# Performance work log

Hardware: AMD Instinct MI355X
Metric: run time of the kernel (lower is better)

Reference implementation:

```python
import jax, jax.numpy as jnp
import numpy as np

B, C, T = 64, 1, 262144
NUM_BANDS = 6
# (min, max) for each of the 18 normalized control params: 6 bands x (gain_dB, cutoff_Hz, Q)
PARAM_RANGES = np.array([
    [-24.0, 24.0], [20.0, 200.0], [0.1, 10.0],      # low shelf
    [-24.0, 24.0], [200.0, 2000.0], [0.1, 10.0],    # band 1
    [-24.0, 24.0], [200.0, 2000.0], [0.1, 10.0],    # band 2
    [-24.0, 24.0], [2000.0, 8000.0], [0.1, 10.0],   # band 3
    [-24.0, 24.0], [4000.0, 12000.0], [0.1, 10.0],  # band 4
    [-24.0, 24.0], [4000.0, 12000.0], [0.1, 10.0],  # high shelf
], dtype=np.float32)
FILTER_TYPES = ["low_shelf", "peaking", "peaking", "peaking", "peaking", "high_shelf"]


def biquad_coeffs(gain_dB, cutoff, q, sr, ftype):
    # Audio-EQ-cookbook biquad coefficients; all inputs shape (B,)
    A = 10.0 ** (gain_dB / 40.0)
    w0 = 2.0 * jnp.pi * (cutoff / sr)
    alpha = jnp.sin(w0) / (2.0 * q)
    c = jnp.cos(w0)
    sA = jnp.sqrt(A)
    if ftype == "low_shelf":
        b0 = A * ((A + 1) - (A - 1) * c + 2 * sA * alpha)
        b1 = 2 * A * ((A - 1) - (A + 1) * c)
        b2 = A * ((A + 1) - (A - 1) * c - 2 * sA * alpha)
        a0 = (A + 1) + (A - 1) * c + 2 * sA * alpha
        a1 = -2 * ((A - 1) + (A + 1) * c)
        a2 = (A + 1) + (A - 1) * c - 2 * sA * alpha
    elif ftype == "high_shelf":
        b0 = A * ((A + 1) + (A - 1) * c + 2 * sA * alpha)
        b1 = -2 * A * ((A - 1) + (A + 1) * c)
        b2 = A * ((A + 1) + (A - 1) * c - 2 * sA * alpha)
        a0 = (A + 1) - (A - 1) * c + 2 * sA * alpha
        a1 = 2 * ((A - 1) - (A + 1) * c)
        a2 = (A + 1) - (A - 1) * c - 2 * sA * alpha
    else:  # peaking
        b0 = 1 + alpha * A
        b1 = -2 * c
        b2 = 1 - alpha * A
        a0 = 1 + alpha / A
        a1 = -2 * c
        a2 = 1 - alpha / A
    bcoef = jnp.stack([b0, b1, b2], axis=-1) / a0[..., None]  # (B, 3)
    acoef = jnp.stack([a0, a1, a2], axis=-1) / a0[..., None]  # (B, 3)
    return bcoef, acoef


def cascade_biquads(x, bcoefs, acoefs):
    # x: (N, T); bcoefs/acoefs: (6, N, 3). Fused cascade of 6 biquads,
    # direct form II transposed, single scan over time.
    def step(state, xt):  # state: (6, N, 2); xt: (N,)
        v = xt
        new_states = []
        for k in range(NUM_BANDS):
            bk, ak = bcoefs[k], acoefs[k]
            s1, s2 = state[k, :, 0], state[k, :, 1]
            y = bk[:, 0] * v + s1
            ns1 = bk[:, 1] * v - ak[:, 1] * y + s2
            ns2 = bk[:, 2] * v - ak[:, 2] * y
            new_states.append(jnp.stack([ns1, ns2], axis=-1))
            v = y
        return jnp.stack(new_states, axis=0), v
    init = jnp.zeros((NUM_BANDS, x.shape[0], 2), dtype=x.dtype)
    _, y = jax.lax.scan(step, init, x.T)  # y: (T, N)
    return y.T


def setup_inputs() -> dict:
    key = jax.random.key(0)
    k1, k2, k3 = jax.random.split(key, 3)
    x = jax.random.normal(k1, (B, C, T), dtype=jnp.float32) * 0.1
    p = jax.random.normal(k2, (B, 22), dtype=jnp.float32)
    W = jax.random.normal(k3, (18, 22), dtype=jnp.float32) * (1.0 / np.sqrt(22.0))
    b = jnp.zeros((18,), dtype=jnp.float32)
    return {"x": x, "p": p, "W": W, "b": b, "sample_rate": 24000}


def reference(x, p, W, b, sample_rate):
    bs, chs, s = x.shape
    sr = jnp.float32(sample_rate)
    # control path: linear + sigmoid -> 18 normalized params in [0, 1]
    pn = jax.nn.sigmoid(p @ W.T + b)  # (bs, 18)
    lo = jnp.asarray(PARAM_RANGES[:, 0])
    hi = jnp.asarray(PARAM_RANGES[:, 1])
    params = pn * (hi - lo) + lo  # denormalized, (bs, 18)
    bcoefs, acoefs = [], []
    for k, ftype in enumerate(FILTER_TYPES):
        g, f, q = params[:, 3 * k], params[:, 3 * k + 1], params[:, 3 * k + 2]
        bk, ak = biquad_coeffs(g, f, q, sr, ftype)
        bcoefs.append(bk)
        acoefs.append(ak)
    bcoefs = jnp.stack(bcoefs, axis=0)  # (6, bs, 3)
    acoefs = jnp.stack(acoefs, axis=0)
    # share each item's EQ across its channels
    bcoefs = jnp.repeat(bcoefs, chs, axis=1)  # (6, bs*chs, 3)
    acoefs = jnp.repeat(acoefs, chs, axis=1)
    y = cascade_biquads(x.reshape(bs * chs, s), bcoefs, acoefs)
    return y.reshape(bs, chs, s)
```

## Files before the change

kernel.cpp:

```cpp
#include <hip/hip_runtime.h>
#include <math.h>

#define NB    64
#define NT    262144
#define CH    64
#define NCK   (NT/CH)
#define NBANDS 6

#define COEF_OFF 0
#define MAT_OFF  4096
#define T_OFF    (MAT_OFF + NB*1728)
#define WPRE_OFF (T_OFF + NB*64*12)
#define D_OFF    (WPRE_OFF + NB*64*12)

struct Coef { float b0, b1, b2, a1, a2; };

__device__ __forceinline__ float rfl(float x) {
  return __int_as_float(__builtin_amdgcn_readfirstlane(__float_as_int(x)));
}

__device__ __forceinline__ float cascade_step(float v, float s[12], const Coef cf[NBANDS]) {
#pragma unroll
  for (int k = 0; k < NBANDS; ++k) {
    float s1 = s[2*k], s2 = s[2*k+1];
    float y   = fmaf(cf[k].b0, v, s1);
    float ns1 = fmaf(cf[k].b1, v, fmaf(-cf[k].a1, y, s2));
    float ns2 = fmaf(cf[k].b2, v, -cf[k].a2 * y);
    s[2*k]   = ns1;
    s[2*k+1] = ns2;
    v = y;
  }
  return v;
}

__device__ __forceinline__ void load_coefs(const float* ws, int batch, Coef cf[NBANDS]) {
  const float* c = ws + COEF_OFF + batch*30;
#pragma unroll
  for (int k = 0; k < NBANDS; ++k) {
    cf[k].b0 = rfl(c[5*k+0]); cf[k].b1 = rfl(c[5*k+1]); cf[k].b2 = rfl(c[5*k+2]);
    cf[k].a1 = rfl(c[5*k+3]); cf[k].a2 = rfl(c[5*k+4]);
  }
}

__global__ __launch_bounds__(64) void k_prep(const float* __restrict__ p, const float* __restrict__ W,
                                             const float* __restrict__ bias, const int* __restrict__ srp,
                                             float* __restrict__ ws) {
  __shared__ float prmS[18];
  __shared__ float cfS[30];
  __shared__ float M0[144], M1[144];
  int b = blockIdx.x, tid = threadIdx.x;
  const float lo[18] = {-24.f,20.f,0.1f,  -24.f,200.f,0.1f,  -24.f,200.f,0.1f,
                        -24.f,2000.f,0.1f, -24.f,4000.f,0.1f, -24.f,4000.f,0.1f};
  const float hi[18] = { 24.f,200.f,10.f,  24.f,2000.f,10.f,  24.f,2000.f,10.f,
                         24.f,8000.f,10.f, 24.f,12000.f,10.f, 24.f,12000.f,10.f};
  if (tid < 18) {
    float acc = bias[tid];
    for (int j = 0; j < 22; ++j) acc = fmaf(W[tid*22+j], p[b*22+j], acc);
    float sg = 1.f / (1.f + expf(-acc));
    prmS[tid] = sg * (hi[tid] - lo[tid]) + lo[tid];
  }
  __syncthreads();
  if (tid < 6) {
    int k = tid;
    float g = prmS[3*k], f = prmS[3*k+1], q = prmS[3*k+2];
    float sr = (float)srp[0];
    float A  = powf(10.f, g * (1.f/40.f));
    float w0 = 6.28318530717958647692f * (f / sr);
    float al = sinf(w0) / (2.f*q);
    float c  = cosf(w0);
    float sA = sqrtf(A);
    float b0,b1,b2,a0,a1,a2;
    if (k == 0) {
      b0 = A*((A+1.f) - (A-1.f)*c + 2.f*sA*al);
      b1 = 2.f*A*((A-1.f) - (A+1.f)*c);
      b2 = A*((A+1.f) - (A-1.f)*c - 2.f*sA*al);
      a0 = (A+1.f) + (A-1.f)*c + 2.f*sA*al;
      a1 = -2.f*((A-1.f) + (A+1.f)*c);
      a2 = (A+1.f) + (A-1.f)*c - 2.f*sA*al;
    } else if (k == 5) {
      b0 = A*((A+1.f) + (A-1.f)*c + 2.f*sA*al);
      b1 = -2.f*A*((A-1.f) + (A+1.f)*c);
      b2 = A*((A+1.f) + (A-1.f)*c - 2.f*sA*al);
      a0 = (A+1.f) - (A-1.f)*c + 2.f*sA*al;
      a1 = 2.f*((A-1.f) - (A+1.f)*c);
      a2 = (A+1.f) - (A-1.f)*c - 2.f*sA*al;
    } else {
      b0 = 1.f + al*A;
      b1 = -2.f*c;
      b2 = 1.f - al*A;
      a0 = 1.f + al/A;
      a1 = -2.f*c;
      a2 = 1.f - al/A;
    }
    float inv = 1.f/a0;
    float* cws = ws + COEF_OFF + b*30;
    cws[5*k+0] = cfS[5*k+0] = b0*inv;
    cws[5*k+1] = cfS[5*k+1] = b1*inv;
    cws[5*k+2] = cfS[5*k+2] = b2*inv;
    cws[5*k+3] = cfS[5*k+3] = a1*inv;
    cws[5*k+4] = cfS[5*k+4] = a2*inv;
  }
  __syncthreads();

  Coef cf[NBANDS];
#pragma unroll
  for (int k = 0; k < NBANDS; ++k) {
    cf[k].b0 = cfS[5*k+0]; cf[k].b1 = cfS[5*k+1]; cf[k].b2 = cfS[5*k+2];
    cf[k].a1 = cfS[5*k+3]; cf[k].a2 = cfS[5*k+4];
  }
  if (tid < 12) {
    float s[12];
#pragma unroll
    for (int r = 0; r < 12; ++r) s[r] = (r == tid) ? 1.f : 0.f;
    cascade_step(0.f, s, cf);
#pragma unroll
    for (int r = 0; r < 12; ++r) M0[r*12 + tid] = s[r];
  }
  __syncthreads();

  float w[12];
#pragma unroll
  for (int r = 0; r < 12; ++r) w[r] = 0.f;
  cascade_step(1.f, w, cf);
  int e63 = 63 - tid;

  float* S = M0; float* D = M1;
  float* mout = ws + MAT_OFF + (size_t)b*1728;
  for (int q = 0; q < 6; ++q) {
    if ((e63 >> q) & 1) {
      float t[12];
#pragma unroll
      for (int r = 0; r < 12; ++r) {
        float acc = 0.f;
#pragma unroll
        for (int k = 0; k < 12; ++k) acc = fmaf(S[r*12+k], w[k], acc);
        t[r] = acc;
      }
#pragma unroll
      for (int r = 0; r < 12; ++r) w[r] = t[r];
    }
    for (int e = tid; e < 144; e += 64) {
      int r = e/12, c = e%12;
      float acc = 0.f;
#pragma unroll
      for (int k = 0; k < 12; ++k) acc = fmaf(S[r*12+k], S[k*12+c], acc);
      D[e] = acc;
    }
    __syncthreads();
    float* t = S; S = D; D = t;
  }
  {
    float* vout = ws + WPRE_OFF + (size_t)b*768;
#pragma unroll
    for (int r = 0; r < 12; ++r) vout[tid*12 + r] = w[r];
  }
  for (int e = tid; e < 144; e += 64) mout[e] = S[e];
  for (int l = 1; l < 12; ++l) {
    for (int e = tid; e < 144; e += 64) {
      int r = e/12, c = e%12;
      float acc = 0.f;
#pragma unroll
      for (int k = 0; k < 12; ++k) acc = fmaf(S[r*12+k], S[k*12+c], acc);
      D[e] = acc;
    }
    __syncthreads();
    float* t = S; S = D; D = t;
    for (int e = tid; e < 144; e += 64) mout[l*144 + e] = S[e];
  }
}

__global__ __launch_bounds__(256, 4) void k_passA(const float* __restrict__ x,
                                                  const float* __restrict__ Vt,
                                                  float* __restrict__ ws) {
  __shared__ float KM[6][144];
  int tid = threadIdx.x, wib = tid >> 6, lane = tid & 63;
  int gw = blockIdx.x*4 + wib;
  int batch = gw >> 6, wv = gw & 63;
  int batch_b = blockIdx.x >> 4;

  const float* mb = ws + MAT_OFF + (size_t)batch_b*1728;
  for (int e = tid; e < 864; e += 256) KM[e/144][e%144] = mb[e];
  __syncthreads();

  const float4* xp = (const float4*)x + (size_t)batch*65536 + (size_t)wv*1024 + (size_t)lane*16;
  const float* Vb = Vt + (size_t)batch_b*768;

  int ph = ((wib << 2) + blockIdx.x) & 15;

  float4 bufs[4];
#pragma unroll
  for (int k = 0; k < 4; ++k) bufs[k] = xp[(ph + k) & 15];

  float s[12];
#pragma unroll
  for (int r = 0; r < 12; ++r) s[r] = 0.f;

#pragma unroll
  for (int j = 0; j < 16; ++j) {
    float4 xv = bufs[j & 3];
    if (j < 12) bufs[j & 3] = xp[(ph + j + 4) & 15];
    int ko = __builtin_amdgcn_readfirstlane(((ph + j) & 15) * 48);
    const float* vr = Vb + ko;
#pragma unroll
    for (int r = 0; r < 12; ++r) {
      float acc = s[r];
      acc = fmaf(vr[r],      xv.x, acc);
      acc = fmaf(vr[12 + r], xv.y, acc);
      acc = fmaf(vr[24 + r], xv.z, acc);
      acc = fmaf(vr[36 + r], xv.w, acc);
      s[r] = acc;
    }
  }

#pragma unroll
  for (int l = 0; l < 6; ++l) {
    const int pd = 1 << l;
    float nb[12];
#pragma unroll
    for (int r = 0; r < 12; ++r) nb[r] = __shfl_up(s[r], pd);
    if (lane >= pd) {
#pragma unroll
      for (int r = 0; r < 12; ++r) {
        float acc = s[r];
#pragma unroll
        for (int c = 0; c < 12; ++c) acc = fmaf(KM[l][r*12+c], nb[c], acc);
        s[r] = acc;
      }
    }
  }

  if (lane == 63) {
    float4* tp = (float4*)(ws + T_OFF + ((size_t)batch*64 + wv)*12);
    tp[0] = make_float4(s[0], s[1], s[2],  s[3]);
    tp[1] = make_float4(s[4], s[5], s[6],  s[7]);
    tp[2] = make_float4(s[8], s[9], s[10], s[11]);
  }

  float e[12];
#pragma unroll
  for (int r = 0; r < 12; ++r) e[r] = __shfl_up(s[r], 1);
  if (lane == 0) {
#pragma unroll
    for (int r = 0; r < 12; ++r) e[r] = 0.f;
  }
  int chunk = wv*64 + lane;
  float4* dp = (float4*)(ws + D_OFF + ((size_t)batch*NCK + chunk)*12);
  dp[0] = make_float4(e[0], e[1], e[2],  e[3]);
  dp[1] = make_float4(e[4], e[5], e[6],  e[7]);
  dp[2] = make_float4(e[8], e[9], e[10], e[11]);
}

__global__ __launch_bounds__(64) void k_scanW(float* __restrict__ ws) {
  __shared__ float WM[6][144];
  int b = blockIdx.x, lane = threadIdx.x;
  const float* mb = ws + MAT_OFF + (size_t)b*1728 + 864;
  for (int e = lane; e < 864; e += 64) WM[e/144][e%144] = mb[e];
  __syncthreads();

  const float4* tp = (const float4*)(ws + T_OFF + ((size_t)b*64 + lane)*12);
  float4 a0 = tp[0], a1 = tp[1], a2 = tp[2];
  float s[12] = {a0.x,a0.y,a0.z,a0.w, a1.x,a1.y,a1.z,a1.w, a2.x,a2.y,a2.z,a2.w};

#pragma unroll
  for (int l = 0; l < 6; ++l) {
    const int pd = 1 << l;
    float nb[12];
#pragma unroll
    for (int r = 0; r < 12; ++r) nb[r] = __shfl_up(s[r], pd);
    if (lane >= pd) {
#pragma unroll
      for (int r = 0; r < 12; ++r) {
        float acc = s[r];
#pragma unroll
        for (int c = 0; c < 12; ++c) acc = fmaf(WM[l][r*12+c], nb[c], acc);
        s[r] = acc;
      }
    }
  }
  float e[12];
#pragma unroll
  for (int r = 0; r < 12; ++r) e[r] = __shfl_up(s[r], 1);
  if (lane == 0) {
#pragma unroll
    for (int r = 0; r < 12; ++r) e[r] = 0.f;
  }
  float4* wp = (float4*)(ws + WPRE_OFF + ((size_t)b*64 + lane)*12);
  wp[0] = make_float4(e[0], e[1], e[2],  e[3]);
  wp[1] = make_float4(e[4], e[5], e[6],  e[7]);
  wp[2] = make_float4(e[8], e[9], e[10], e[11]);
}

__global__ __launch_bounds__(256) void k_passB(const float* __restrict__ x, const float* __restrict__ ws,
                                               float* __restrict__ out) {
  __shared__ float4 buf[4][2][256];
  __shared__ float KM[6][144];
  int tid = threadIdx.x, wib = tid >> 6, lane = tid & 63;
  int gw = blockIdx.x*4 + wib;
  int batch = gw >> 6, wv = gw & 63;
  int batch_b = blockIdx.x >> 4;

  const float* mb = ws + MAT_OFF + (size_t)batch_b*1728;
  for (int e = tid; e < 864; e += 256) KM[e/144][e%144] = mb[e];
  __syncthreads();

  const float4* x4 = (const float4*)x;
  float4* out4 = (float4*)out;
  size_t gbase4 = (size_t)batch*65536 + (size_t)wv*1024;
  int r2 = lane >> 2, c2 = lane & 3;
  float4* bufA = buf[wib][0];
  float4* bufB = buf[wib][1];

  float4 va[4], vb[4];
#pragma unroll
  for (int j = 0; j < 4; ++j) va[j] = x4[gbase4 + (size_t)(j*16 + r2)*16 + c2];

  Coef cf[NBANDS];
  load_coefs(ws, batch, cf);

  int chunk = wv*64 + lane;
  const float4* dp = (const float4*)(ws + D_OFF + ((size_t)batch*NCK + chunk)*12);
  float4 e0 = dp[0], e1 = dp[1], e2 = dp[2];
  const float4* wp = (const float4*)(ws + WPRE_OFF + ((size_t)batch*64 + wv)*12);
  float4 w0 = wp[0], w1 = wp[1], w2 = wp[2];
  float R[12] = {w0.x,w0.y,w0.z,w0.w, w1.x,w1.y,w1.z,w1.w, w2.x,w2.y,w2.z,w2.w};
#pragma unroll
  for (int l = 0; l < 6; ++l) {
    float t[12];
#pragma unroll
    for (int r = 0; r < 12; ++r) {
      float acc = 0.f;
#pragma unroll
      for (int c = 0; c < 12; ++c) acc = fmaf(KM[l][r*12+c], R[c], acc);
      t[r] = acc;
    }
    bool sel = (lane >> l) & 1;
#pragma unroll
    for (int r = 0; r < 12; ++r) R[r] = sel ? t[r] : R[r];
  }
  float s[12] = {e0.x+R[0], e0.y+R[1], e0.z+R[2],  e0.w+R[3],
                 e1.x+R[4], e1.y+R[5], e1.z+R[6],  e1.w+R[7],
                 e2.x+R[8], e2.y+R[9], e2.z+R[10], e2.w+R[11]};

#pragma unroll
  for (int j = 0; j < 4; ++j) bufA[c2*64 + j*16 + r2] = va[j];
  asm volatile("s_waitcnt lgkmcnt(0)" ::: "memory");

#pragma unroll
  for (int q = 0; q < 4; ++q) {
    float4* bp = (q & 1) ? bufB : bufA;
    float4* bn = (q & 1) ? bufA : bufB;
    float4* vr = (q & 1) ? va : vb;
    if (q < 3) {
#pragma unroll
      for (int j = 0; j < 4; ++j)
        vr[j] = x4[gbase4 + (size_t)(j*16 + r2)*16 + (q+1)*4 + c2];
    }
#pragma unroll
    for (int t = 0; t < 4; ++t) {
      float4 xv = bp[t*64 + lane];
      float4 yv;
      yv.x = cascade_step(xv.x, s, cf);
      yv.y = cascade_step(xv.y, s, cf);
      yv.z = cascade_step(xv.z, s, cf);
      yv.w = cascade_step(xv.w, s, cf);
      bp[t*64 + lane] = yv;
    }
    asm volatile("s_waitcnt lgkmcnt(0)" ::: "memory");
#pragma unroll
    for (int j = 0; j < 4; ++j) {
      float4 w = bp[c2*64 + j*16 + r2];
      out4[gbase4 + (size_t)(j*16 + r2)*16 + q*4 + c2] = w;
    }
    if (q < 3) {
#pragma unroll
      for (int j = 0; j < 4; ++j) bn[c2*64 + j*16 + r2] = vr[j];
      asm volatile("s_waitcnt lgkmcnt(0)" ::: "memory");
    }
  }
}

extern "C" void kernel_launch(void* const* d_in, const int* in_sizes, int n_in,
                              void* d_out, int out_size, void* d_ws, size_t ws_size,
                              hipStream_t stream) {
  const float* x    = (const float*)d_in[0];
  const float* p    = (const float*)d_in[1];
  const float* W    = (const float*)d_in[2];
  const float* bias = (const float*)d_in[3];
  const int*   sr   = (const int*)d_in[4];
  float* ws  = (float*)d_ws;
  float* out = (float*)d_out;

  int passBlocks = (NB * NCK) / 256;
  hipLaunchKernelGGL(k_prep,  dim3(NB),         dim3(64),  0, stream, p, W, bias, sr, ws);
  hipLaunchKernelGGL(k_passA, dim3(passBlocks), dim3(256), 0, stream, x, ws + WPRE_OFF, ws);
  hipLaunchKernelGGL(k_scanW, dim3(NB),         dim3(64),  0, stream, ws);
  hipLaunchKernelGGL(k_passB, dim3(passBlocks), dim3(256), 0, stream, x, ws, out);
}
```

Before: 98.32 us.

## Fold warp-level scan into passB and stream passA input via global_load_lds ring

Removes the separate k_scanW launch: each passB wavefront redoes the 64-lane 12x12 matrix prefix scan over the per-warp totals and picks its predecessor's prefix with a shuffle. This needs the second half of the matrix table in LDS. passA now streams its input through a per-wave LDS ring filled by direct global-to-LDS loads, with explicit vmcnt waits, instead of a rotated-phase register buffer. The intent is to save one kernel launch and its dependency gap and to deepen load pipelining, at the cost of redundant scan arithmetic in every passB wave and more LDS per block.

Measured after the change: 101.5 us. 1.03x slower.

```diff
diff --git a/kernel.cpp b/kernel.cpp
--- a/kernel.cpp
+++ b/kernel.cpp
@@ -10,13 +10,26 @@
 #define COEF_OFF 0
 #define MAT_OFF  4096
 #define T_OFF    (MAT_OFF + NB*1728)
-#define WPRE_OFF (T_OFF + NB*64*12)
-#define D_OFF    (WPRE_OFF + NB*64*12)
+#define V_OFF    (T_OFF + NB*64*12)
+#define D_OFF    (V_OFF + NB*64*12)
 
 struct Coef { float b0, b1, b2, a1, a2; };
 
 __device__ __forceinline__ float rfl(float x) {
   return __int_as_float(__builtin_amdgcn_readfirstlane(__float_as_int(x)));
+}
+
+__device__ __forceinline__ void wait_vmcnt(int n) {
+  switch (n) {
+    case 0: asm volatile("s_waitcnt vmcnt(0)" ::: "memory"); break;
+    case 1: asm volatile("s_waitcnt vmcnt(1)" ::: "memory"); break;
+    case 2: asm volatile("s_waitcnt vmcnt(2)" ::: "memory"); break;
+    case 3: asm volatile("s_waitcnt vmcnt(3)" ::: "memory"); break;
+    case 4: asm volatile("s_waitcnt vmcnt(4)" ::: "memory"); break;
+    case 5: asm volatile("s_waitcnt vmcnt(5)" ::: "memory"); break;
+    case 6: asm volatile("s_waitcnt vmcnt(6)" ::: "memory"); break;
+    default: asm volatile("s_waitcnt vmcnt(7)" ::: "memory"); break;
+  }
 }
 
 __device__ __forceinline__ float cascade_step(float v, float s[12], const Coef cf[NBANDS]) {
@@ -150,7 +163,7 @@
     float* t = S; S = D; D = t;
   }
   {
-    float* vout = ws + WPRE_OFF + (size_t)b*768;
+    float* vout = ws + V_OFF + (size_t)b*768;
 #pragma unroll
     for (int r = 0; r < 12; ++r) vout[tid*12 + r] = w[r];
   }
@@ -173,6 +186,7 @@
                                                   const float* __restrict__ Vt,
                                                   float* __restrict__ ws) {
   __shared__ float KM[6][144];
+  __shared__ float4 ring[4][8][64];
   int tid = threadIdx.x, wib = tid >> 6, lane = tid & 63;
   int gw = blockIdx.x*4 + wib;
   int batch = gw >> 6, wv = gw & 63;
@@ -182,25 +196,31 @@
   for (int e = tid; e < 864; e += 256) KM[e/144][e%144] = mb[e];
   __syncthreads();
 
-  const float4* xp = (const float4*)x + (size_t)batch*65536 + (size_t)wv*1024 + (size_t)lane*16;
+  const float4* xg = (const float4*)x + (size_t)batch*65536 + (size_t)wv*1024 + (size_t)lane*16;
   const float* Vb = Vt + (size_t)batch_b*768;
 
-  int ph = ((wib << 2) + blockIdx.x) & 15;
-
-  float4 bufs[4];
-#pragma unroll
-  for (int k = 0; k < 4; ++k) bufs[k] = xp[(ph + k) & 15];
+#pragma unroll
+  for (int g = 0; g < 8; ++g) {
+    __builtin_amdgcn_global_load_lds(
+        (const __attribute__((address_space(1))) void*)(xg + g),
+        (__attribute__((address_space(3))) void*)&ring[wib][g][0], 16, 0, 0);
+  }
 
   float s[12];
 #pragma unroll
   for (int r = 0; r < 12; ++r) s[r] = 0.f;
 
 #pragma unroll
-  for (int j = 0; j < 16; ++j) {
-    float4 xv = bufs[j & 3];
-    if (j < 12) bufs[j & 3] = xp[(ph + j + 4) & 15];
-    int ko = __builtin_amdgcn_readfirstlane(((ph + j) & 15) * 48);
-    const float* vr = Vb + ko;
+  for (int g = 0; g < 16; ++g) {
+    wait_vmcnt((g < 8) ? 7 : (15 - g));
+    float4 xv = ring[wib][g & 7][lane];
+    asm volatile("s_waitcnt lgkmcnt(0)" ::: "memory");
+    if (g < 8) {
+      __builtin_amdgcn_global_load_lds(
+          (const __attribute__((address_space(1))) void*)(xg + (g + 8)),
+          (__attribute__((address_space(3))) void*)&ring[wib][g][0], 16, 0, 0);
+    }
+    const float* vr = Vb + g*48;
 #pragma unroll
     for (int r = 0; r < 12; ++r) {
       float acc = s[r];
@@ -250,57 +270,17 @@
   dp[2] = make_float4(e[8], e[9], e[10], e[11]);
 }
 
-__global__ __launch_bounds__(64) void k_scanW(float* __restrict__ ws) {
-  __shared__ float WM[6][144];
-  int b = blockIdx.x, lane = threadIdx.x;
-  const float* mb = ws + MAT_OFF + (size_t)b*1728 + 864;
-  for (int e = lane; e < 864; e += 64) WM[e/144][e%144] = mb[e];
-  __syncthreads();
-
-  const float4* tp = (const float4*)(ws + T_OFF + ((size_t)b*64 + lane)*12);
-  float4 a0 = tp[0], a1 = tp[1], a2 = tp[2];
-  float s[12] = {a0.x,a0.y,a0.z,a0.w, a1.x,a1.y,a1.z,a1.w, a2.x,a2.y,a2.z,a2.w};
-
-#pragma unroll
-  for (int l = 0; l < 6; ++l) {
-    const int pd = 1 << l;
-    float nb[12];
-#pragma unroll
-    for (int r = 0; r < 12; ++r) nb[r] = __shfl_up(s[r], pd);
-    if (lane >= pd) {
-#pragma unroll
-      for (int r = 0; r < 12; ++r) {
-        float acc = s[r];
-#pragma unroll
-        for (int c = 0; c < 12; ++c) acc = fmaf(WM[l][r*12+c], nb[c], acc);
-        s[r] = acc;
-      }
-    }
-  }
-  float e[12];
-#pragma unroll
-  for (int r = 0; r < 12; ++r) e[r] = __shfl_up(s[r], 1);
-  if (lane == 0) {
-#pragma unroll
-    for (int r = 0; r < 12; ++r) e[r] = 0.f;
-  }
-  float4* wp = (float4*)(ws + WPRE_OFF + ((size_t)b*64 + lane)*12);
-  wp[0] = make_float4(e[0], e[1], e[2],  e[3]);
-  wp[1] = make_float4(e[4], e[5], e[6],  e[7]);
-  wp[2] = make_float4(e[8], e[9], e[10], e[11]);
-}
-
 __global__ __launch_bounds__(256) void k_passB(const float* __restrict__ x, const float* __restrict__ ws,
                                                float* __restrict__ out) {
   __shared__ float4 buf[4][2][256];
-  __shared__ float KM[6][144];
+  __shared__ float KM[12][144];
   int tid = threadIdx.x, wib = tid >> 6, lane = tid & 63;
   int gw = blockIdx.x*4 + wib;
   int batch = gw >> 6, wv = gw & 63;
   int batch_b = blockIdx.x >> 4;
 
   const float* mb = ws + MAT_OFF + (size_t)batch_b*1728;
-  for (int e = tid; e < 864; e += 256) KM[e/144][e%144] = mb[e];
+  for (int e = tid; e < 1728; e += 256) KM[e/144][e%144] = mb[e];
   __syncthreads();
 
   const float4* x4 = (const float4*)x;
@@ -320,9 +300,34 @@
   int chunk = wv*64 + lane;
   const float4* dp = (const float4*)(ws + D_OFF + ((size_t)batch*NCK + chunk)*12);
   float4 e0 = dp[0], e1 = dp[1], e2 = dp[2];
-  const float4* wp = (const float4*)(ws + WPRE_OFF + ((size_t)batch*64 + wv)*12);
-  float4 w0 = wp[0], w1 = wp[1], w2 = wp[2];
-  float R[12] = {w0.x,w0.y,w0.z,w0.w, w1.x,w1.y,w1.z,w1.w, w2.x,w2.y,w2.z,w2.w};
+  const float4* tp = (const float4*)(ws + T_OFF + ((size_t)batch*64 + lane)*12);
+  float4 t0 = tp[0], t1 = tp[1], t2 = tp[2];
+
+  float sc[12] = {t0.x,t0.y,t0.z,t0.w, t1.x,t1.y,t1.z,t1.w, t2.x,t2.y,t2.z,t2.w};
+#pragma unroll
+  for (int l = 0; l < 6; ++l) {
+    const int pd = 1 << l;
+    float nb[12];
+#pragma unroll
+    for (int r = 0; r < 12; ++r) nb[r] = __shfl_up(sc[r], pd);
+    if (lane >= pd) {
+#pragma unroll
+      for (int r = 0; r < 12; ++r) {
+        float acc = sc[r];
+#pragma unroll
+        for (int c = 0; c < 12; ++c) acc = fmaf(KM[6+l][r*12+c], nb[c], acc);
+        sc[r] = acc;
+      }
+    }
+  }
+  int bsrc = (wv == 0) ? 0 : (wv - 1);
+  float R[12];
+#pragma unroll
+  for (int r = 0; r < 12; ++r) R[r] = __shfl(sc[r], bsrc);
+  if (wv == 0) {
+#pragma unroll
+    for (int r = 0; r < 12; ++r) R[r] = 0.f;
+  }
 #pragma unroll
   for (int l = 0; l < 6; ++l) {
     float t[12];
@@ -392,7 +397,6 @@
 
   int passBlocks = (NB * NCK) / 256;
   hipLaunchKernelGGL(k_prep,  dim3(NB),         dim3(64),  0, stream, p, W, bias, sr, ws);
-  hipLaunchKernelGGL(k_passA, dim3(passBlocks), dim3(256), 0, stream, x, ws + WPRE_OFF, ws);
-  hipLaunchKernelGGL(k_scanW, dim3(NB),         dim3(64),  0, stream, ws);
+  hipLaunchKernelGGL(k_passA, dim3(passBlocks), dim3(256), 0, stream, x, ws + V_OFF, ws);
   hipLaunchKernelGGL(k_passB, dim3(passBlocks), dim3(256), 0, stream, x, ws, out);
 }
```
